# Kernel tuning notes

Measured on AMD Instinct MI355X. Metric: run time of the kernel, lower is better.

Reference implementation:

```python
import jax, jax.numpy as jnp
import numpy as np

B, LA, LQ, LO, H, OUT = 32, 2048, 64, 32, 1024, 5


def _kaiming(key, out_f, in_f):
    return jax.random.normal(key, (out_f, in_f), jnp.float32) * np.sqrt(2.0 / in_f)


def setup_inputs() -> dict:
    key = jax.random.key(0)
    ks = jax.random.split(key, 16)
    inp = {
        "article_contexts": jax.random.normal(ks[0], (B, LA, H), jnp.float32),
        "question_contexts": jax.random.normal(ks[1], (B, LQ, H), jnp.float32),
        "options_embeds": jax.random.normal(ks[2], (B, 5, LO, H), jnp.float32),
        "answer_indices": jax.random.randint(ks[3], (B,), 0, LQ),
    }
    # mlp_att (article-question attention) params
    inp["a_Qw"], inp["a_Qb"] = _kaiming(ks[4], H, H), jnp.zeros((H,), jnp.float32)
    inp["a_Kw"], inp["a_Kb"] = _kaiming(ks[5], H, H), jnp.zeros((H,), jnp.float32)
    inp["a_Vw"], inp["a_Vb"] = _kaiming(ks[6], H, H), jnp.zeros((H,), jnp.float32)
    inp["a_vw"], inp["a_vb"] = _kaiming(ks[7], 1, H), jnp.zeros((1,), jnp.float32)
    # dot_layer (option attention) params
    inp["d_Qw"], inp["d_Qb"] = _kaiming(ks[8], H, H), jnp.zeros((H,), jnp.float32)
    inp["d_Kw"], inp["d_Kb"] = _kaiming(ks[9], H, H), jnp.zeros((H,), jnp.float32)
    inp["d_Vw"], inp["d_Vb"] = _kaiming(ks[10], H, H), jnp.zeros((H,), jnp.float32)
    inp["d_vw"], inp["d_vb"] = _kaiming(ks[11], 1, H), jnp.zeros((1,), jnp.float32)
    # final linear: hidden_size*5 -> output_dim
    inp["f_w"], inp["f_b"] = _kaiming(ks[12], OUT, 5 * H), jnp.zeros((OUT,), jnp.float32)
    return inp


def _mlp_att(Q, K, V, Qw, Qb, Kw, Kb, Vw, Vb, vw, vb):
    # Q: [B, H]; K, V: [B, (..opt..), L, H]. Dropout is identity (eval mode).
    Qp = Q @ Qw.T + Qb                      # [B, H]
    Kp = K @ Kw.T + Kb                      # [..., L, H]
    Vp = V @ Vw.T + Vb                      # [..., L, H]
    while Qp.ndim < Kp.ndim:
        Qp = Qp[..., None, :]
    M = jnp.tanh(Qp + Kp)                   # [..., L, H]
    scores = jax.nn.softmax(M @ vw.T + vb, axis=-2)  # softmax over L, [..., L, 1]
    return jnp.sum(Vp * scores, axis=-2)    # [..., H]


def reference(article_contexts, question_contexts, options_embeds, answer_indices,
              a_Qw, a_Qb, a_Kw, a_Kb, a_Vw, a_Vb, a_vw, a_vb,
              d_Qw, d_Qb, d_Kw, d_Kb, d_Vw, d_Vb, d_vw, d_vb,
              f_w, f_b):
    b = article_contexts.shape[0]
    # gather question context at the answer index -> [B, H]
    oqc = question_contexts[jnp.arange(b), answer_indices]
    # article-question additive attention -> [B, H]
    aq = _mlp_att(oqc, article_contexts, article_contexts,
                  a_Qw, a_Qb, a_Kw, a_Kb, a_Vw, a_Vb, a_vw, a_vb)
    # per-option additive attention, vectorized over the 5 options -> [B, 5, H]
    feats = _mlp_att(aq, options_embeds, options_embeds,
                     d_Qw, d_Qb, d_Kw, d_Kb, d_Vw, d_Vb, d_vw, d_vb)
    # concat options along feature dim, final linear -> [B, OUT]
    logits = feats.reshape(b, -1) @ f_w.T + f_b
    return logits
```

## Files before the change

### kernel.cpp

```cpp
#include <hip/hip_runtime.h>
#include <hip/hip_bf16.h>
#include <math.h>

#define HDIM 1024
#define NB 32
#define LA 2048
#define LO 32

typedef __attribute__((ext_vector_type(8))) short bf16x8;
typedef __attribute__((ext_vector_type(4))) float f32x4;
typedef unsigned int u32;

__device__ __forceinline__ float tanh_fast(float x){
    return 2.0f / (1.0f + __expf(-2.0f * x)) - 1.0f;
}

__device__ __forceinline__ void load_lds16(const void* gptr, void* lptr){
    __builtin_amdgcn_global_load_lds(
        (const __attribute__((address_space(1))) u32*)gptr,
        (__attribute__((address_space(3))) u32*)lptr, 16, 0, 0);
}

__global__ void zero_kernel(float* __restrict__ p, int n){
    int i = blockIdx.x * blockDim.x + threadIdx.x;
    int stride = gridDim.x * blockDim.x;
    for (; i < n; i += stride) p[i] = 0.0f;
}

__global__ void conv_bf16_kernel(const float* __restrict__ in, __hip_bfloat16* __restrict__ out, long n){
    long i = ((long)blockIdx.x * blockDim.x + threadIdx.x) * 4;
    long stride = (long)gridDim.x * blockDim.x * 4;
    for (; i < n; i += stride){
        float4 v = *(const float4*)(in + i);
        union { __hip_bfloat16 h[4]; short4 s; } u;
        u.h[0] = __float2bfloat16(v.x); u.h[1] = __float2bfloat16(v.y);
        u.h[2] = __float2bfloat16(v.z); u.h[3] = __float2bfloat16(v.w);
        *(short4*)(out + i) = u.s;
    }
}

__global__ void conv2_bf16_kernel(const float* __restrict__ in0, __hip_bfloat16* __restrict__ out0, long n0,
                                  const float* __restrict__ in1, __hip_bfloat16* __restrict__ out1, long n1){
    const float* in; __hip_bfloat16* out; long n; long base;
    if (blockIdx.x < 64){ in = in0; out = out0; n = n0; base = (long)blockIdx.x; 
        long i = (base * blockDim.x + threadIdx.x) * 4;
        long stride = 64L * blockDim.x * 4;
        for (; i < n; i += stride){
            float4 v = *(const float4*)(in + i);
            union { __hip_bfloat16 h[4]; short4 s; } u;
            u.h[0] = __float2bfloat16(v.x); u.h[1] = __float2bfloat16(v.y);
            u.h[2] = __float2bfloat16(v.z); u.h[3] = __float2bfloat16(v.w);
            *(short4*)(out + i) = u.s;
        }
    } else { in = in1; out = out1; n = n1; base = (long)(blockIdx.x - 64);
        long i = (base * blockDim.x + threadIdx.x) * 4;
        long stride = 320L * blockDim.x * 4;
        for (; i < n; i += stride){
            float4 v = *(const float4*)(in + i);
            union { __hip_bfloat16 h[4]; short4 s; } u;
            u.h[0] = __float2bfloat16(v.x); u.h[1] = __float2bfloat16(v.y);
            u.h[2] = __float2bfloat16(v.z); u.h[3] = __float2bfloat16(v.w);
            *(short4*)(out + i) = u.s;
        }
    }
}

__global__ __launch_bounds__(256) void proj_q_kernel(
    const float* __restrict__ question, const int* __restrict__ ans,
    const float* __restrict__ W, const float* __restrict__ bias, float* __restrict__ out){
    __shared__ float xin[HDIM];
    const int g = blockIdx.x, tid = threadIdx.x;
    const int lane = tid & 63, wave = tid >> 6;
    const float* in = question + ((size_t)g * 64 + ans[g]) * HDIM;
    *(float4*)&xin[tid * 4] = *(const float4*)&in[tid * 4];
    __syncthreads();
    float4 xv[4];
    #pragma unroll
    for (int c = 0; c < 4; c++) xv[c] = *(const float4*)&xin[(c * 64 + lane) * 4];
    const int hbase = blockIdx.y * 64 + wave * 16;
    #pragma unroll 4
    for (int r = 0; r < 16; r++){
        int h = hbase + r;
        const float* Wr = W + (size_t)h * HDIM;
        float p = 0.f;
        #pragma unroll
        for (int c = 0; c < 4; c++){
            float4 wv = *(const float4*)&Wr[(c * 64 + lane) * 4];
            p = fmaf(xv[c].x, wv.x, p); p = fmaf(xv[c].y, wv.y, p);
            p = fmaf(xv[c].z, wv.z, p); p = fmaf(xv[c].w, wv.w, p);
        }
        #pragma unroll
        for (int off = 1; off < 64; off <<= 1) p += __shfl_xor(p, off, 64);
        if (lane == 0) out[(size_t)g * HDIM + h] = p + bias[h];
    }
}

__global__ __launch_bounds__(256) void proj_kernel(
    const float* __restrict__ in, const float* __restrict__ W,
    const float* __restrict__ bias, float* __restrict__ out){
    __shared__ float xin[HDIM];
    const int g = blockIdx.x, tid = threadIdx.x;
    const int lane = tid & 63, wave = tid >> 6;
    *(float4*)&xin[tid * 4] = *(const float4*)&in[(size_t)g * HDIM + tid * 4];
    __syncthreads();
    float4 xv[4];
    #pragma unroll
    for (int c = 0; c < 4; c++) xv[c] = *(const float4*)&xin[(c * 64 + lane) * 4];
    const int hbase = blockIdx.y * 64 + wave * 16;
    #pragma unroll 4
    for (int r = 0; r < 16; r++){
        int h = hbase + r;
        const float* Wr = W + (size_t)h * HDIM;
        float p = 0.f;
        #pragma unroll
        for (int c = 0; c < 4; c++){
            float4 wv = *(const float4*)&Wr[(c * 64 + lane) * 4];
            p = fmaf(xv[c].x, wv.x, p); p = fmaf(xv[c].y, wv.y, p);
            p = fmaf(xv[c].z, wv.z, p); p = fmaf(xv[c].w, wv.w, p);
        }
        #pragma unroll
        for (int off = 1; off < 64; off <<= 1) p += __shfl_xor(p, off, 64);
        if (lane == 0) out[(size_t)g * HDIM + h] = p + bias[h];
    }
}

#define NTT 16
__global__ __launch_bounds__(512, 2) void score_mfma8p(
    const __hip_bfloat16* __restrict__ X, const __hip_bfloat16* __restrict__ Kw,
    const float* __restrict__ Kb, const float* __restrict__ Qp,
    const float* __restrict__ vw, float* __restrict__ s,
    int rows_per_batch)
{
    __shared__ __align__(16) char lds[131072];
    const int tid = threadIdx.x;
    const int lane = tid & 63, wid = tid >> 6;
    const int wm = wid >> 2, wn = wid & 3;
    const int lr = lane & 15, lg = lane >> 4;

    const int na = gridDim.x >> 2;
    const int bid = blockIdx.x;
    const int xcd = bid & 7, seq = bid >> 3;
    const int a_idx = xcd * (na >> 3) + (seq >> 2);
    const int h_idx = seq & 3;
    const int a0 = a_idx * 256, h0 = h_idx * 256;

    f32x4 acc[8][4] = {};
    bf16x8 av[8], bv[4];

    const int rA = tid >> 2;
    const int csw = ((tid & 3) * 16) ^ (((rA >> 1) & 3) << 4);
    const char* pA = (const char*)Kw + (size_t)(h0 + rA) * 2048 + csw;
    const char* pB = (const char*)X  + (size_t)(a0 + rA) * 2048 + csw;
    char* dst0 = lds + tid * 16;

    int aoff[8], boff[4];
    #pragma unroll
    for (int hf = 0; hf < 8; hf++){
        int rw = wm * 128 + hf * 16 + lr;
        aoff[hf] = rw * 64 + ((lg * 16) ^ (((rw >> 1) & 3) << 4));
    }
    #pragma unroll
    for (int af = 0; af < 4; af++){
        int rw = wn * 64 + af * 16 + lr;
        boff[af] = 16384 + rw * 64 + ((lg * 16) ^ (((rw >> 1) & 3) << 4));
    }

#define ISSUE(P, KOFF, SLOT, PLANE) do { \
    load_lds16((P) + (KOFF), dst0 + (SLOT) + (PLANE)); \
    load_lds16((P) + (KOFF) + 262144, dst0 + (SLOT) + (PLANE) + 8192); } while(0)
#define READS_A(BASE) do { \
    _Pragma("unroll") \
    for (int hf = 0; hf < 8; hf++) av[hf] = *(const bf16x8*)(lds + (BASE) + aoff[hf]); \
    bv[0] = *(const bf16x8*)(lds + (BASE) + boff[0]); \
    bv[1] = *(const bf16x8*)(lds + (BASE) + boff[1]); } while(0)
#define READS_B(BASE) do { \
    bv[2] = *(const bf16x8*)(lds + (BASE) + boff[2]); \
    bv[3] = *(const bf16x8*)(lds + (BASE) + boff[3]); } while(0)
#define MFMA2(A0, A1) do { __builtin_amdgcn_s_setprio(1); \
    _Pragma("unroll") \
    for (int hf = 0; hf < 8; hf++){ \
        acc[hf][A0] = __builtin_amdgcn_mfma_f32_16x16x32_bf16(av[hf], bv[A0], acc[hf][A0], 0, 0, 0); \
        acc[hf][A1] = __builtin_amdgcn_mfma_f32_16x16x32_bf16(av[hf], bv[A1], acc[hf][A1], 0, 0, 0); } \
    __builtin_amdgcn_s_setprio(0); } while(0)
#define BAR() __builtin_amdgcn_s_barrier()

    ISSUE(pA, 0, 0, 0);        ISSUE(pB, 0, 0, 16384);
    ISSUE(pA, 64, 0, 32768);   ISSUE(pB, 64, 0, 49152);
    ISSUE(pA, 128, 65536, 0);  ISSUE(pB, 128, 65536, 16384);

    for (int t = 0; t < 14; ++t){
        const int st = (t & 1) << 16;
        const int so = st ^ 65536;
        const int kb = t * 128;
        ISSUE(pA, kb + 192, so, 32768);
        asm volatile("s_waitcnt vmcnt(10)" ::: "memory");
        BAR();
        READS_A(st);
        BAR();
        MFMA2(0, 1);
        ISSUE(pB, kb + 192, so, 49152);
        READS_B(st);
        BAR();
        MFMA2(2, 3);
        ISSUE(pA, kb + 256, st, 0);
        asm volatile("s_waitcnt vmcnt(10)" ::: "memory");
        BAR();
        READS_A(st + 32768);
        BAR();
        MFMA2(0, 1);
        ISSUE(pB, kb + 256, st, 16384);
        READS_B(st + 32768);
        BAR();
        MFMA2(2, 3);
    }
    {
        ISSUE(pA, 14 * 128 + 192, 65536, 32768);
        asm volatile("s_waitcnt vmcnt(10)" ::: "memory");
        BAR(); READS_A(0); BAR(); MFMA2(0, 1);
        ISSUE(pB, 14 * 128 + 192, 65536, 49152);
        READS_B(0); BAR(); MFMA2(2, 3);
        asm volatile("s_waitcnt vmcnt(8)" ::: "memory");
        BAR(); READS_A(32768); BAR(); MFMA2(0, 1);
        READS_B(32768); BAR(); MFMA2(2, 3);
    }
    {
        asm volatile("s_waitcnt vmcnt(4)" ::: "memory");
        BAR(); READS_A(65536); BAR(); MFMA2(0, 1);
        READS_B(65536); BAR(); MFMA2(2, 3);
        asm volatile("s_waitcnt vmcnt(0)" ::: "memory");
        BAR(); READS_A(65536 + 32768); BAR(); MFMA2(0, 1);
        READS_B(65536 + 32768); BAR(); MFMA2(2, 3);
    }

    const int b = a0 / rows_per_batch;
    float part[4] = {0.f, 0.f, 0.f, 0.f};
    #pragma unroll
    for (int hf = 0; hf < 8; hf++){
        int hbase = h0 + wm * 128 + hf * 16 + lg * 4;
        float4 kb4 = *(const float4*)(Kb + hbase);
        float4 qp4 = *(const float4*)(Qp + (size_t)b * HDIM + hbase);
        float4 vw4 = *(const float4*)(vw + hbase);
        float q0v = kb4.x + qp4.x, q1v = kb4.y + qp4.y;
        float q2v = kb4.z + qp4.z, q3v = kb4.w + qp4.w;
        #pragma unroll
        for (int af = 0; af < 4; af++){
            part[af] += tanh_fast(acc[hf][af][0] + q0v) * vw4.x;
            part[af] += tanh_fast(acc[hf][af][1] + q1v) * vw4.y;
            part[af] += tanh_fast(acc[hf][af][2] + q2v) * vw4.z;
            part[af] += tanh_fast(acc[hf][af][3] + q3v) * vw4.w;
        }
    }
    #pragma unroll
    for (int af = 0; af < 4; af++){
        float p = part[af];
        p += __shfl_xor(p, 16, 64);
        p += __shfl_xor(p, 32, 64);
        if (lane < 16)
            atomicAdd(&s[a0 + wn * 64 + af * 16 + lr], p);
    }
#undef ISSUE
#undef READS_A
#undef READS_B
#undef MFMA2
#undef BAR
}

#define SBM 128
#define SBN 128
__global__ __launch_bounds__(256) void score_mfma_kernel(
    const __hip_bfloat16* __restrict__ X, const __hip_bfloat16* __restrict__ Kw,
    const float* __restrict__ Kb, const float* __restrict__ Qp,
    const float* __restrict__ vw, float* __restrict__ s,
    int row_off, int rows_per_batch)
{
    __shared__ __align__(16) __hip_bfloat16 As[SBM][32];
    __shared__ __align__(16) __hip_bfloat16 Bs[SBN][32];
    const int tid = threadIdx.x;
    const int lane = tid & 63, wid = tid >> 6;
    const int wm = wid >> 1, wn = wid & 1;
    const int row0 = blockIdx.x * SBM;
    const int h0 = blockIdx.y * SBN;
    const int lr = lane & 15, lg = lane >> 4;

    f32x4 acc[4][4] = {};

    for (int k0 = 0; k0 < HDIM; k0 += 32){
        #pragma unroll
        for (int l = 0; l < 2; l++){
            int f = tid + l * 256;
            int r = f >> 2, c8 = (f & 3) * 8;
            load_lds16(X + (size_t)(row0 + r) * HDIM + k0 + c8, &As[0][0] + f * 8);
            load_lds16(Kw + (size_t)(h0 + r) * HDIM + k0 + c8, &Bs[0][0] + f * 8);
        }
        __syncthreads();
        bf16x8 a[4], b[4];
        #pragma unroll
        for (int i = 0; i < 4; i++)
            a[i] = *(const bf16x8*)&As[wm * 64 + i * 16 + lr][lg * 8];
        #pragma unroll
        for (int j = 0; j < 4; j++)
            b[j] = *(const bf16x8*)&Bs[wn * 64 + j * 16 + lr][lg * 8];
        #pragma unroll
        for (int i = 0; i < 4; i++)
            #pragma unroll
            for (int j = 0; j < 4; j++)
                acc[i][j] = __builtin_amdgcn_mfma_f32_16x16x32_bf16(a[i], b[j], acc[i][j], 0, 0, 0);
        __syncthreads();
    }

    float kbv[4], vwv[4];
    #pragma unroll
    for (int j = 0; j < 4; j++){
        int h = h0 + wn * 64 + j * 16 + lr;
        kbv[j] = Kb[h]; vwv[j] = vw[h];
    }
    #pragma unroll
    for (int i = 0; i < 4; i++){
        #pragma unroll
        for (int reg = 0; reg < 4; reg++){
            int r = row0 + wm * 64 + i * 16 + lg * 4 + reg;
            int gr = row_off + r;
            int bb = gr / rows_per_batch;
            const float* Qpb = Qp + (size_t)bb * HDIM;
            float p = 0.f;
            #pragma unroll
            for (int j = 0; j < 4; j++){
                int h = h0 + wn * 64 + j * 16 + lr;
                p += tanh_fast(acc[i][j][reg] + kbv[j] + Qpb[h]) * vwv[j];
            }
            #pragma unroll
            for (int off = 1; off < 16; off <<= 1) p += __shfl_xor(p, off, 16);
            if (lr == 0) atomicAdd(&s[gr], p);
        }
    }
}

__global__ void softmax_kernel(float* __restrict__ s, int Rg){
    __shared__ float red[4];
    int g = blockIdx.x, tid = threadIdx.x;
    float* sg = s + (size_t)g * Rg;
    float m = -INFINITY;
    for (int i = tid; i < Rg; i += 256) m = fmaxf(m, sg[i]);
    #pragma unroll
    for (int off = 32; off > 0; off >>= 1) m = fmaxf(m, __shfl_down(m, off, 64));
    if ((tid & 63) == 0) red[tid >> 6] = m;
    __syncthreads();
    m = fmaxf(fmaxf(red[0], red[1]), fmaxf(red[2], red[3]));
    __syncthreads();
    float sum = 0.f;
    for (int i = tid; i < Rg; i += 256){ float e = __expf(sg[i] - m); sg[i] = e; sum += e; }
    #pragma unroll
    for (int off = 32; off > 0; off >>= 1) sum += __shfl_down(sum, off, 64);
    if ((tid & 63) == 0) red[tid >> 6] = sum;
    __syncthreads();
    float inv = 1.0f / (red[0] + red[1] + red[2] + red[3]);
    for (int i = tid; i < Rg; i += 256) sg[i] *= inv;
}

__global__ __launch_bounds__(256) void wsum_art_v(
    const __hip_bfloat16* __restrict__ X, const float* __restrict__ sc,
    float* __restrict__ out){
    __shared__ float scs[256];
    const int g = blockIdx.x, ic = blockIdx.y, tid = threadIdx.x;
    scs[tid] = sc[(size_t)g * LA + ic * 256 + tid];
    __syncthreads();
    const __hip_bfloat16* Xg = X + ((size_t)g * LA + ic * 256) * HDIM + tid * 4;
    float a0 = 0.f, a1 = 0.f, a2 = 0.f, a3 = 0.f;
    for (int i = 0; i < 256; i++){
        short4 v = *(const short4*)(Xg + (size_t)i * HDIM);
        float w = scs[i];
        a0 = fmaf(w, __bfloat162float(*(const __hip_bfloat16*)&v.x), a0);
        a1 = fmaf(w, __bfloat162float(*(const __hip_bfloat16*)&v.y), a1);
        a2 = fmaf(w, __bfloat162float(*(const __hip_bfloat16*)&v.z), a2);
        a3 = fmaf(w, __bfloat162float(*(const __hip_bfloat16*)&v.w), a3);
    }
    float* o = out + (size_t)g * HDIM + tid * 4;
    atomicAdd(o + 0, a0); atomicAdd(o + 1, a1);
    atomicAdd(o + 2, a2); atomicAdd(o + 3, a3);
}

__global__ __launch_bounds__(256) void wsum_opt_v(
    const __hip_bfloat16* __restrict__ X, const float* __restrict__ sc,
    float* __restrict__ out){
    __shared__ float scs[LO];
    const int g = blockIdx.x, tid = threadIdx.x;
    if (tid < LO) scs[tid] = sc[(size_t)g * LO + tid];
    __syncthreads();
    const __hip_bfloat16* Xg = X + (size_t)g * LO * HDIM + tid * 4;
    float a0 = 0.f, a1 = 0.f, a2 = 0.f, a3 = 0.f;
    for (int i = 0; i < LO; i++){
        short4 v = *(const short4*)(Xg + (size_t)i * HDIM);
        float w = scs[i];
        a0 = fmaf(w, __bfloat162float(*(const __hip_bfloat16*)&v.x), a0);
        a1 = fmaf(w, __bfloat162float(*(const __hip_bfloat16*)&v.y), a1);
        a2 = fmaf(w, __bfloat162float(*(const __hip_bfloat16*)&v.z), a2);
        a3 = fmaf(w, __bfloat162float(*(const __hip_bfloat16*)&v.w), a3);
    }
    float* o = out + (size_t)g * HDIM + tid * 4;
    o[0] = a0; o[1] = a1; o[2] = a2; o[3] = a3;
}

__global__ void final_kernel(const float* __restrict__ feats, const float* __restrict__ fw,
                             const float* __restrict__ fb, float* __restrict__ out){
    __shared__ float red[4];
    int b = blockIdx.x, tid = threadIdx.x;
    const float* fe = feats + (size_t)b * 5120;
    for (int j = 0; j < 5; j++){
        float acc = 0.f;
        for (int i = tid; i < 5120; i += 256) acc += fe[i] * fw[(size_t)j * 5120 + i];
        #pragma unroll
        for (int off = 32; off > 0; off >>= 1) acc += __shfl_down(acc, off, 64);
        if ((tid & 63) == 0) red[tid >> 6] = acc;
        __syncthreads();
        if (tid == 0) out[b * 5 + j] = fb[j] + red[0] + red[1] + red[2] + red[3];
        __syncthreads();
    }
}

extern "C" void kernel_launch(void* const* d_in, const int* in_sizes, int n_in,
                              void* d_out, int out_size, void* d_ws, size_t ws_size,
                              hipStream_t stream) {
    const float* article  = (const float*)d_in[0];
    const float* question = (const float*)d_in[1];
    const float* options  = (const float*)d_in[2];
    const int*   ans      = (const int*)d_in[3];
    const float* a_Qw = (const float*)d_in[4];  const float* a_Qb = (const float*)d_in[5];
    const float* a_Kw = (const float*)d_in[6];  const float* a_Kb = (const float*)d_in[7];
    const float* a_Vw = (const float*)d_in[8];  const float* a_Vb = (const float*)d_in[9];
    const float* a_vw = (const float*)d_in[10];
    const float* d_Qw = (const float*)d_in[12]; const float* d_Qb = (const float*)d_in[13];
    const float* d_Kw = (const float*)d_in[14]; const float* d_Kb = (const float*)d_in[15];
    const float* d_Vw = (const float*)d_in[16]; const float* d_Vb = (const float*)d_in[17];
    const float* d_vw = (const float*)d_in[18];
    const float* f_w  = (const float*)d_in[20]; const float* f_b  = (const float*)d_in[21];
    float* out = (float*)d_out;

    float* ws = (float*)d_ws;
    float* qp_a  = ws + 32768;
    float* aq    = ws + 65536;
    float* qp_d  = ws + 98304;
    float* feats = ws + 131072;
    float* s_art = ws + 294912;
    float* s_opt = ws + 360448;
    float* w_art = ws + 365568;
    float* wd    = ws + 398336;
    __hip_bfloat16* kwa_bf = (__hip_bfloat16*)(ws + 562176);
    __hip_bfloat16* kwd_bf = kwa_bf + 1048576;
    __hip_bfloat16* opt_bf = kwd_bf + 1048576;
    __hip_bfloat16* art_bf = opt_bf + 5242880;

    zero_kernel<<<128, 256, 0, stream>>>(s_art, 103424);
    proj_q_kernel<<<dim3(NB, 16), 256, 0, stream>>>(question, ans, a_Qw, a_Qb, qp_a);
    conv_bf16_kernel<<<64, 256, 0, stream>>>(a_Kw, kwa_bf, 1048576);
    conv_bf16_kernel<<<1024, 256, 0, stream>>>(article, art_bf, (long)NB * LA * HDIM);

    score_mfma8p<<<(NB * LA / 256) * 4, 512, 0, stream>>>(
        art_bf, kwa_bf, a_Kb, qp_a, a_vw, s_art, LA);
    softmax_kernel<<<NB, 256, 0, stream>>>(s_art, LA);
    wsum_art_v<<<dim3(NB, 8), 256, 0, stream>>>(art_bf, s_art, w_art);
    proj_kernel<<<dim3(NB, 16), 256, 0, stream>>>(w_art, a_Vw, a_Vb, aq);

    proj_kernel<<<dim3(NB, 16), 256, 0, stream>>>(aq, d_Qw, d_Qb, qp_d);
    conv2_bf16_kernel<<<384, 256, 0, stream>>>(d_Kw, kwd_bf, 1048576,
                                               options, opt_bf, 5242880);
    score_mfma_kernel<<<dim3((NB * 5 * LO) / SBM, HDIM / SBN), 256, 0, stream>>>(
        opt_bf, kwd_bf, d_Kb, qp_d, d_vw, s_opt, 0, 5 * LO);
    softmax_kernel<<<NB * 5, 256, 0, stream>>>(s_opt, LO);
    wsum_opt_v<<<NB * 5, 256, 0, stream>>>(opt_bf, s_opt, wd);
    proj_kernel<<<dim3(NB * 5, 16), 256, 0, stream>>>(wd, d_Vw, d_Vb, feats);
    final_kernel<<<NB, 256, 0, stream>>>(feats, f_w, f_b, out);
}
```

Measured before the change: 425.5 us.

## Restructure score GEMM pipeline into 4-stage ring with one barrier per k-step

Replaces the hand-interleaved double-buffered main loop of the MFMA scoring kernel with a uniform 4-slot ring. Each k-step waits on outstanding loads, issues one barrier, prefetches 3 stages ahead, reads all A/B fragments and runs 32 MFMAs. The aim is to cut the barrier count per k-step from three to one and give the scheduler a simpler, deeper prefetch pipeline. The risk is a possible WAR hazard on the slot being refilled, since the prefetch is issued right after a single barrier, and the longer MFMA burst may expose more LDS latency. The conv kernel edit is a cosmetic cleanup.

```diff
diff --git a/kernel.cpp b/kernel.cpp
--- a/kernel.cpp
+++ b/kernel.cpp
@@ -41,26 +41,25 @@
 
 __global__ void conv2_bf16_kernel(const float* __restrict__ in0, __hip_bfloat16* __restrict__ out0, long n0,
                                   const float* __restrict__ in1, __hip_bfloat16* __restrict__ out1, long n1){
-    const float* in; __hip_bfloat16* out; long n; long base;
-    if (blockIdx.x < 64){ in = in0; out = out0; n = n0; base = (long)blockIdx.x; 
-        long i = (base * blockDim.x + threadIdx.x) * 4;
+    if (blockIdx.x < 64){
+        long i = ((long)blockIdx.x * blockDim.x + threadIdx.x) * 4;
         long stride = 64L * blockDim.x * 4;
-        for (; i < n; i += stride){
-            float4 v = *(const float4*)(in + i);
+        for (; i < n0; i += stride){
+            float4 v = *(const float4*)(in0 + i);
             union { __hip_bfloat16 h[4]; short4 s; } u;
             u.h[0] = __float2bfloat16(v.x); u.h[1] = __float2bfloat16(v.y);
             u.h[2] = __float2bfloat16(v.z); u.h[3] = __float2bfloat16(v.w);
-            *(short4*)(out + i) = u.s;
-        }
-    } else { in = in1; out = out1; n = n1; base = (long)(blockIdx.x - 64);
-        long i = (base * blockDim.x + threadIdx.x) * 4;
+            *(short4*)(out0 + i) = u.s;
+        }
+    } else {
+        long i = ((long)(blockIdx.x - 64) * blockDim.x + threadIdx.x) * 4;
         long stride = 320L * blockDim.x * 4;
-        for (; i < n; i += stride){
-            float4 v = *(const float4*)(in + i);
+        for (; i < n1; i += stride){
+            float4 v = *(const float4*)(in1 + i);
             union { __hip_bfloat16 h[4]; short4 s; } u;
             u.h[0] = __float2bfloat16(v.x); u.h[1] = __float2bfloat16(v.y);
             u.h[2] = __float2bfloat16(v.z); u.h[3] = __float2bfloat16(v.w);
-            *(short4*)(out + i) = u.s;
+            *(short4*)(out1 + i) = u.s;
         }
     }
 }
@@ -124,7 +123,6 @@
     }
 }
 
-#define NTT 16
 __global__ __launch_bounds__(512, 2) void score_mfma8p(
     const __hip_bfloat16* __restrict__ X, const __hip_bfloat16* __restrict__ Kw,
     const float* __restrict__ Kb, const float* __restrict__ Qp,
@@ -165,71 +163,59 @@
         boff[af] = 16384 + rw * 64 + ((lg * 16) ^ (((rw >> 1) & 3) << 4));
     }
 
-#define ISSUE(P, KOFF, SLOT, PLANE) do { \
-    load_lds16((P) + (KOFF), dst0 + (SLOT) + (PLANE)); \
-    load_lds16((P) + (KOFF) + 262144, dst0 + (SLOT) + (PLANE) + 8192); } while(0)
-#define READS_A(BASE) do { \
+#define ISSUE_PAIR(j) do { \
+    const int _base = (((j) >> 1) & 1) * 65536 + ((j) & 1) * 32768; \
+    const size_t _ko = (size_t)(((j) >> 1) * 128 + ((j) & 1) * 64); \
+    load_lds16(pA + _ko, dst0 + _base); \
+    load_lds16(pA + _ko + 262144, dst0 + _base + 8192); \
+    load_lds16(pB + _ko, dst0 + _base + 16384); \
+    load_lds16(pB + _ko + 262144, dst0 + _base + 24576); } while(0)
+
+#define READS_PAIR(k) do { \
+    const int _base = (((k) >> 1) & 1) * 65536 + ((k) & 1) * 32768; \
     _Pragma("unroll") \
-    for (int hf = 0; hf < 8; hf++) av[hf] = *(const bf16x8*)(lds + (BASE) + aoff[hf]); \
-    bv[0] = *(const bf16x8*)(lds + (BASE) + boff[0]); \
-    bv[1] = *(const bf16x8*)(lds + (BASE) + boff[1]); } while(0)
-#define READS_B(BASE) do { \
-    bv[2] = *(const bf16x8*)(lds + (BASE) + boff[2]); \
-    bv[3] = *(const bf16x8*)(lds + (BASE) + boff[3]); } while(0)
-#define MFMA2(A0, A1) do { __builtin_amdgcn_s_setprio(1); \
+    for (int hf = 0; hf < 8; hf++) av[hf] = *(const bf16x8*)(lds + _base + aoff[hf]); \
     _Pragma("unroll") \
-    for (int hf = 0; hf < 8; hf++){ \
-        acc[hf][A0] = __builtin_amdgcn_mfma_f32_16x16x32_bf16(av[hf], bv[A0], acc[hf][A0], 0, 0, 0); \
-        acc[hf][A1] = __builtin_amdgcn_mfma_f32_16x16x32_bf16(av[hf], bv[A1], acc[hf][A1], 0, 0, 0); } \
+    for (int af = 0; af < 4; af++) bv[af] = *(const bf16x8*)(lds + _base + boff[af]); } while(0)
+
+#define MFMA32() do { \
+    asm volatile("s_waitcnt lgkmcnt(0)" ::: "memory"); \
+    __builtin_amdgcn_sched_barrier(0); \
+    __builtin_amdgcn_s_setprio(1); \
+    _Pragma("unroll") \
+    for (int hf = 0; hf < 8; hf++) \
+        _Pragma("unroll") \
+        for (int af = 0; af < 4; af++) \
+            acc[hf][af] = __builtin_amdgcn_mfma_f32_16x16x32_bf16(av[hf], bv[af], acc[hf][af], 0, 0, 0); \
     __builtin_amdgcn_s_setprio(0); } while(0)
-#define BAR() __builtin_amdgcn_s_barrier()
-
-    ISSUE(pA, 0, 0, 0);        ISSUE(pB, 0, 0, 16384);
-    ISSUE(pA, 64, 0, 32768);   ISSUE(pB, 64, 0, 49152);
-    ISSUE(pA, 128, 65536, 0);  ISSUE(pB, 128, 65536, 16384);
-
-    for (int t = 0; t < 14; ++t){
-        const int st = (t & 1) << 16;
-        const int so = st ^ 65536;
-        const int kb = t * 128;
-        ISSUE(pA, kb + 192, so, 32768);
-        asm volatile("s_waitcnt vmcnt(10)" ::: "memory");
-        BAR();
-        READS_A(st);
-        BAR();
-        MFMA2(0, 1);
-        ISSUE(pB, kb + 192, so, 49152);
-        READS_B(st);
-        BAR();
-        MFMA2(2, 3);
-        ISSUE(pA, kb + 256, st, 0);
-        asm volatile("s_waitcnt vmcnt(10)" ::: "memory");
-        BAR();
-        READS_A(st + 32768);
-        BAR();
-        MFMA2(0, 1);
-        ISSUE(pB, kb + 256, st, 16384);
-        READS_B(st + 32768);
-        BAR();
-        MFMA2(2, 3);
+
+    ISSUE_PAIR(0); ISSUE_PAIR(1); ISSUE_PAIR(2);
+
+    #pragma unroll 2
+    for (int k = 0; k < 29; ++k){
+        asm volatile("s_waitcnt vmcnt(8)" ::: "memory");
+        __builtin_amdgcn_s_barrier();
+        ISSUE_PAIR(k + 3);
+        READS_PAIR(k);
+        MFMA32();
     }
     {
-        ISSUE(pA, 14 * 128 + 192, 65536, 32768);
-        asm volatile("s_waitcnt vmcnt(10)" ::: "memory");
-        BAR(); READS_A(0); BAR(); MFMA2(0, 1);
-        ISSUE(pB, 14 * 128 + 192, 65536, 49152);
-        READS_B(0); BAR(); MFMA2(2, 3);
         asm volatile("s_waitcnt vmcnt(8)" ::: "memory");
-        BAR(); READS_A(32768); BAR(); MFMA2(0, 1);
-        READS_B(32768); BAR(); MFMA2(2, 3);
+        __builtin_amdgcn_s_barrier();
+        READS_PAIR(29);
+        MFMA32();
     }
     {
         asm volatile("s_waitcnt vmcnt(4)" ::: "memory");
-        BAR(); READS_A(65536); BAR(); MFMA2(0, 1);
-        READS_B(65536); BAR(); MFMA2(2, 3);
+        __builtin_amdgcn_s_barrier();
+        READS_PAIR(30);
+        MFMA32();
+    }
+    {
         asm volatile("s_waitcnt vmcnt(0)" ::: "memory");
-        BAR(); READS_A(65536 + 32768); BAR(); MFMA2(0, 1);
-        READS_B(65536 + 32768); BAR(); MFMA2(2, 3);
+        __builtin_amdgcn_s_barrier();
+        READS_PAIR(31);
+        MFMA32();
     }
 
     const int b = a0 / rows_per_batch;
@@ -258,11 +244,9 @@
         if (lane < 16)
             atomicAdd(&s[a0 + wn * 64 + af * 16 + lr], p);
     }
-#undef ISSUE
-#undef READS_A
-#undef READS_B
-#undef MFMA2
-#undef BAR
+#undef ISSUE_PAIR
+#undef READS_PAIR
+#undef MFMA32
 }
 
 #define SBM 128
```

New measurement: 427.6 us. Within noise of the previous version (+0.5%).
